# Performance work log

Hardware: AMD Instinct MI355X
Metric: run time of the kernel (lower is better)

## Reference

```python
import jax, jax.numpy as jnp
import numpy as np

EMBED_DIM = 256
NUM_EMBEDDINGS = 1024
COMMITMENT_COST = 0.25


def setup_inputs() -> dict:
    key = jax.random.key(0)
    k1, k2 = jax.random.split(key)
    z_e = jax.random.normal(k1, (64, 32, 32, EMBED_DIM), dtype=jnp.float32)
    # variance_scaling(fan_in, uniform) ~ U(-sqrt(3/fan_in), sqrt(3/fan_in))
    lim = float(np.sqrt(3.0 / EMBED_DIM))
    codebook = jax.random.uniform(k2, (NUM_EMBEDDINGS, EMBED_DIM), dtype=jnp.float32,
                                  minval=-lim, maxval=lim)
    return {"z_e": z_e, "codebook": codebook}


def reference(z_e, codebook):
    codebook = jnp.asarray(codebook, dtype=jnp.float32)
    z_flat = jnp.reshape(z_e, (-1, codebook.shape[1]))  # [N, D]
    # ||z||^2 - 2 z.c + ||c||^2 -> [N, K]
    distances = (jnp.sum(z_flat ** 2, axis=1, keepdims=True)
                 - 2.0 * jnp.dot(z_flat, codebook.T)
                 + jnp.sum(codebook ** 2, axis=1))
    encoding_indices = jnp.argmin(distances, axis=1)  # [N]
    quantized = jnp.reshape(codebook[encoding_indices], z_e.shape)
    commitment_loss = COMMITMENT_COST * jnp.mean((jax.lax.stop_gradient(quantized) - z_e) ** 2)
    embedding_loss = jnp.mean((quantized - jax.lax.stop_gradient(z_e)) ** 2)
    quantized = z_e + jax.lax.stop_gradient(quantized - z_e)  # straight-through
    return (quantized, commitment_loss, embedding_loss, encoding_indices)
```

## Files before the change

### kernel.cpp

```cpp
#include <hip/hip_runtime.h>

#define NROWS  65536
#define DIM    256
#define KCB    1024
#define DELTA  0.012f
#define DELTA2 2.0e-4f
#define NRMAX  65536
#define REFB   1024

typedef __attribute__((ext_vector_type(8))) _Float16 v8h;
typedef __attribute__((ext_vector_type(4))) float v4f;
typedef __attribute__((ext_vector_type(4))) int   v4i;

__device__ __forceinline__ unsigned short h16(float x) {
  _Float16 h = (_Float16)x;
  return __builtin_bit_cast(unsigned short, h);
}
__device__ __forceinline__ unsigned pk2h(float a, float b) {
  return (unsigned)h16(a) | ((unsigned)h16(b) << 16);
}
__device__ __forceinline__ v4i pk8h(float4 a, float4 b) {
  v4i r; r.x = (int)pk2h(a.x,a.y); r.y = (int)pk2h(a.z,a.w);
  r.z = (int)pk2h(b.x,b.y); r.w = (int)pk2h(b.z,b.w);
  return r;
}
__device__ __forceinline__ float f16f(float x) { return (float)(_Float16)x; }
__device__ __forceinline__ void gld16(const void* g, void* l) {
  __builtin_amdgcn_global_load_lds(
      (const __attribute__((address_space(1))) unsigned int*)g,
      (__attribute__((address_space(3))) unsigned int*)l, 16, 0, 0);
}

__global__ __launch_bounds__(256) void prep_kernel(const float* __restrict__ cb,
                                                   float* __restrict__ cnorm,
                                                   unsigned short* __restrict__ cbh,
                                                   unsigned short* __restrict__ cbl,
                                                   int* __restrict__ cnt,
                                                   int* __restrict__ cnt2) {
  int g = blockIdx.x * 256 + threadIdx.x;
  if (g == 0) { *cnt = 0; *cnt2 = 0; }
  int k = g >> 2, q = g & 3;
  int nt = k >> 7, c = k & 127;
  const float4* row = reinterpret_cast<const float4*>(cb + (size_t)k * DIM) + q * 16;
  size_t off = (size_t)((nt * 4 + q) * 128 + c) * 64;
  unsigned short* dh = cbh + off;
  unsigned short* dl = cbl + off;
  int xr = (c & 7) << 3;
  double s = 0.0;
#pragma unroll
  for (int i = 0; i < 8; ++i) {
    float4 a = row[2 * i], b = row[2 * i + 1];
    s += (double)a.x * a.x + (double)a.y * a.y + (double)a.z * a.z + (double)a.w * a.w;
    s += (double)b.x * b.x + (double)b.y * b.y + (double)b.z * b.z + (double)b.w * b.w;
    *(v4i*)(dh + ((i * 8) ^ xr)) = pk8h(a, b);
    float4 ar, br;
    ar.x = a.x - f16f(a.x); ar.y = a.y - f16f(a.y);
    ar.z = a.z - f16f(a.z); ar.w = a.w - f16f(a.w);
    br.x = b.x - f16f(b.x); br.y = b.y - f16f(b.y);
    br.z = b.z - f16f(b.z); br.w = b.w - f16f(b.w);
    *(v4i*)(dl + ((i * 8) ^ xr)) = pk8h(ar, br);
  }
  s += __shfl_xor(s, 1);
  s += __shfl_xor(s, 2);
  if (q == 0) cnorm[k] = (float)s;
}

__global__ __launch_bounds__(256, 2) void vq_mfma(
    const float* __restrict__ z, const unsigned short* __restrict__ cbh,
    const float* __restrict__ cnw, int* __restrict__ idx_arr,
    int* __restrict__ list, int* __restrict__ cnt) {
  __shared__ __align__(16) short S[32768];

  const int t = threadIdx.x;
  const int l = t & 63;
  const int w = t >> 6;
  const int l15 = l & 15, lhi = l >> 4;
  const int wm = w * 32;
  const int r0 = blockIdx.x * 128;

#pragma unroll
  for (int p = 0; p < 16; ++p) {
    int u = t + p * 256;
    int row = u >> 5, k8 = u & 31;
    const float4* s = (const float4*)(z + (size_t)(r0 + row) * DIM + k8 * 8);
    float4 a = s[0], b = s[1];
    *(v4i*)(S + row * 256 + ((k8 * 8) ^ ((row & 7) << 3))) = pk8h(a, b);
  }
  __syncthreads();

  v8h A[2][8];
#pragma unroll
  for (int mf = 0; mf < 2; ++mf) {
    int arow = wm + mf * 16 + l15;
    int base = arow * 256, xr = (arow & 7) << 3;
#pragma unroll
    for (int ks8 = 0; ks8 < 8; ++ks8)
      A[mf][ks8] = *(const v8h*)(S + base + ((ks8 * 32 + lhi * 8) ^ xr));
  }
  __syncthreads();

  auto stageC = [&](int p) {
    const char* gb = (const char*)cbh + (size_t)p * 32768 + w * 8192 + l * 16;
    char* lb = (char*)(S + (p & 1) * 16384) + w * 8192;
#pragma unroll
    for (int j = 0; j < 8; ++j) gld16(gb + j * 1024, lb + j * 1024);
  };

  int bcode[8], boff[8], bxr[8];
#pragma unroll
  for (int nf = 0; nf < 8; ++nf) {
    bcode[nf] = nf * 16 + l15;
    boff[nf] = bcode[nf] * 64;
    bxr[nf] = (bcode[nf] & 7) << 3;
  }

  float m1[8], m2[8]; int i1[8];
#pragma unroll
  for (int sl = 0; sl < 8; ++sl) { m1[sl] = 3.0e38f; m2[sl] = 3.0e38f; i1[sl] = 0; }

  stageC(0);
  __syncthreads();

  for (int nt = 0; nt < 8; ++nt) {
    float cnv[8];
#pragma unroll
    for (int nf = 0; nf < 8; ++nf) cnv[nf] = cnw[nt * 128 + bcode[nf]];

    v4f acc[2][8];
#pragma unroll
    for (int mf = 0; mf < 2; ++mf)
#pragma unroll
      for (int nf = 0; nf < 8; ++nf) acc[mf][nf] = (v4f){0.f, 0.f, 0.f, 0.f};

    for (int kh = 0; kh < 2; ++kh) {
      int p = nt * 2 + kh;
      if (p < 15) stageC(p + 1);
      const short* cur = S + (p & 1) * 16384;
#pragma unroll
      for (int ks = 0; ks < 4; ++ks) {
        int sub = (ks >> 1) * 8192;
        int ko = (ks & 1) * 32 + lhi * 8;
        v8h b[8];
#pragma unroll
        for (int nf = 0; nf < 8; ++nf)
          b[nf] = *(const v8h*)(cur + sub + boff[nf] + (ko ^ bxr[nf]));
#pragma unroll
        for (int mf = 0; mf < 2; ++mf)
#pragma unroll
          for (int nf = 0; nf < 8; ++nf)
            acc[mf][nf] = __builtin_amdgcn_mfma_f32_16x16x32_f16(A[mf][kh * 4 + ks], b[nf], acc[mf][nf], 0, 0, 0);
      }
      __syncthreads();
    }

#pragma unroll
    for (int mf = 0; mf < 2; ++mf)
#pragma unroll
      for (int nf = 0; nf < 8; ++nf) {
        int code = nt * 128 + bcode[nf];
#pragma unroll
        for (int r = 0; r < 4; ++r) {
          float s = fmaf(-2.f, acc[mf][nf][r], cnv[nf]);
          int sl = mf * 4 + r;
          m2[sl] = fminf(m2[sl], fmaxf(m1[sl], s));
          bool lt = s < m1[sl];
          i1[sl] = lt ? code : i1[sl];
          m1[sl] = lt ? s : m1[sl];
        }
      }
  }

#pragma unroll
  for (int off = 1; off < 16; off <<= 1) {
#pragma unroll
    for (int sl = 0; sl < 8; ++sl) {
      float o1 = __shfl_xor(m1[sl], off);
      int   oi = __shfl_xor(i1[sl], off);
      float o2 = __shfl_xor(m2[sl], off);
      bool bb = (o1 < m1[sl]) || (o1 == m1[sl] && oi < i1[sl]);
      float hi = fmaxf(m1[sl], o1);
      m2[sl] = fminf(hi, fminf(m2[sl], o2));
      m1[sl] = bb ? o1 : m1[sl];
      i1[sl] = bb ? oi : i1[sl];
    }
  }

  if (l15 == 0) {
#pragma unroll
    for (int sl = 0; sl < 8; ++sl) {
      int row = wm + (sl >> 2) * 16 + lhi * 4 + (sl & 3);
      idx_arr[r0 + row] = i1[sl];
      if (m2[sl] - m1[sl] < DELTA) {
        int p = atomicAdd(cnt, 1);
        list[p] = r0 + row;
      }
    }
  }
}

__global__ __launch_bounds__(256, 2) void vq_fused(
    const float* __restrict__ z, const float* __restrict__ cb,
    const unsigned short* __restrict__ cbh, const unsigned short* __restrict__ cbl,
    const float* __restrict__ cnw, const int* __restrict__ list,
    const int* __restrict__ cnt, const int* __restrict__ idx_arr,
    float* __restrict__ pm1, float* __restrict__ pm2, int* __restrict__ pi1,
    float* __restrict__ out_q, float* __restrict__ out_idx,
    float* __restrict__ rowloss) {
  __shared__ __align__(16) short Ch[2][8192];
  __shared__ __align__(16) short Cl[2][8192];
  __shared__ int rows_s[64];
  __shared__ int idxs[16];

  const int t = threadIdx.x;
  const int l = t & 63, w = t >> 6;
  const int l15 = l & 15, lhi = l >> 4;

  if (blockIdx.x < REFB) {
    const int n = *cnt;
    const int ngroups = (n + 63) >> 6;
    const int cq = blockIdx.x & 3;

    auto stage2 = [&](int g, int buf) {
      size_t go = (size_t)g * 16384 + w * 4096 + l * 16;
      char* lh = (char*)Ch[buf] + w * 4096;
      char* ll = (char*)Cl[buf] + w * 4096;
#pragma unroll
      for (int j = 0; j < 4; ++j) gld16((const char*)cbh + go + j * 1024, lh + j * 1024);
#pragma unroll
      for (int j = 0; j < 4; ++j) gld16((const char*)cbl + go + j * 1024, ll + j * 1024);
    };

    const int bxr = (l15 & 7) << 3;

    for (int grp = blockIdx.x >> 2; grp < ngroups; grp += (REFB >> 2)) {
      int base = grp * 64;
      __syncthreads();
      if (t < 64) rows_s[t] = list[min(base + t, n - 1)];
      __syncthreads();
      int rowg = rows_s[w * 16 + l15];

      v8h Ah[8], Al[8];
#pragma unroll
      for (int ks8 = 0; ks8 < 8; ++ks8) {
        const float* p = z + (size_t)rowg * 256 + ks8 * 32 + lhi * 8;
        float4 a = *(const float4*)p, b = *(const float4*)(p + 4);
        v8h hv, lv;
        hv[0] = (_Float16)a.x; lv[0] = (_Float16)(a.x - (float)hv[0]);
        hv[1] = (_Float16)a.y; lv[1] = (_Float16)(a.y - (float)hv[1]);
        hv[2] = (_Float16)a.z; lv[2] = (_Float16)(a.z - (float)hv[2]);
        hv[3] = (_Float16)a.w; lv[3] = (_Float16)(a.w - (float)hv[3]);
        hv[4] = (_Float16)b.x; lv[4] = (_Float16)(b.x - (float)hv[4]);
        hv[5] = (_Float16)b.y; lv[5] = (_Float16)(b.y - (float)hv[5]);
        hv[6] = (_Float16)b.z; lv[6] = (_Float16)(b.z - (float)hv[6]);
        hv[7] = (_Float16)b.w; lv[7] = (_Float16)(b.w - (float)hv[7]);
        Ah[ks8] = hv; Al[ks8] = lv;
      }

      stage2(cq * 8, 0);
      __syncthreads();

      float m1[4], m2[4]; int i1[4];
#pragma unroll
      for (int r = 0; r < 4; ++r) { m1[r] = 3.0e38f; m2[r] = 3.0e38f; i1[r] = 0; }

#pragma unroll
      for (int tnt = 0; tnt < 2; ++tnt) {
        int nt = cq * 2 + tnt;
        float cnv[8];
#pragma unroll
        for (int nf = 0; nf < 8; ++nf) cnv[nf] = cnw[nt * 128 + nf * 16 + l15];

        v4f acc[8];
#pragma unroll
        for (int nf = 0; nf < 8; ++nf) acc[nf] = (v4f){0.f, 0.f, 0.f, 0.f};

        for (int kc = 0; kc < 4; ++kc) {
          int ph = tnt * 4 + kc;
          int g = nt * 4 + kc;
          if (ph < 7) stage2(g + 1, (ph + 1) & 1);
          const short* ch = Ch[ph & 1];
          const short* cl = Cl[ph & 1];
#pragma unroll
          for (int ks = 0; ks < 2; ++ks) {
            int ko = (ks * 32 + lhi * 8) ^ bxr;
            v8h bh[8], bl8[8];
#pragma unroll
            for (int nf = 0; nf < 8; ++nf) {
              int bo = (nf * 16 + l15) * 64 + ko;
              bh[nf]  = *(const v8h*)(ch + bo);
              bl8[nf] = *(const v8h*)(cl + bo);
            }
            v8h ah = Ah[kc * 2 + ks], al = Al[kc * 2 + ks];
#pragma unroll
            for (int nf = 0; nf < 8; ++nf) {
              acc[nf] = __builtin_amdgcn_mfma_f32_16x16x32_f16(al, bh[nf], acc[nf], 0, 0, 0);
              acc[nf] = __builtin_amdgcn_mfma_f32_16x16x32_f16(ah, bl8[nf], acc[nf], 0, 0, 0);
              acc[nf] = __builtin_amdgcn_mfma_f32_16x16x32_f16(ah, bh[nf], acc[nf], 0, 0, 0);
            }
          }
          __syncthreads();
        }

#pragma unroll
        for (int nf = 0; nf < 8; ++nf) {
          int code = nt * 128 + nf * 16 + l15;
#pragma unroll
          for (int r = 0; r < 4; ++r) {
            float s = fmaf(-2.f, acc[nf][r], cnv[nf]);
            m2[r] = fminf(m2[r], fmaxf(m1[r], s));
            bool lt = s < m1[r];
            i1[r] = lt ? code : i1[r];
            m1[r] = lt ? s : m1[r];
          }
        }
      }

#pragma unroll
      for (int off = 1; off < 16; off <<= 1) {
#pragma unroll
        for (int r = 0; r < 4; ++r) {
          float o1 = __shfl_xor(m1[r], off);
          int   oi = __shfl_xor(i1[r], off);
          float o2 = __shfl_xor(m2[r], off);
          bool bb = (o1 < m1[r]) || (o1 == m1[r] && oi < i1[r]);
          float hi = fmaxf(m1[r], o1);
          m2[r] = fminf(hi, fminf(m2[r], o2));
          m1[r] = bb ? o1 : m1[r];
          i1[r] = bb ? oi : i1[r];
        }
      }

      if (l15 == 0) {
#pragma unroll
        for (int r = 0; r < 4; ++r) {
          int fr = w * 16 + lhi * 4 + r;
          int pos = base + fr;
          if (pos < n) {
            pm1[cq * NRMAX + pos] = m1[r];
            pm2[cq * NRMAX + pos] = m2[r];
            pi1[cq * NRMAX + pos] = i1[r];
          }
        }
      }
    }
  } else {
    const int b0 = (blockIdx.x - REFB) * 16;
    if (t < 16) {
      int k = idx_arr[b0 + t];
      idxs[t] = k;
      out_idx[b0 + t] = (float)k;
    }
    __syncthreads();
    const float4* zb = (const float4*)(z + (size_t)b0 * DIM);
    float4* qb = (float4*)(out_q + (size_t)b0 * DIM);
#pragma unroll
    for (int p = 0; p < 4; ++p) {
      int rl = p * 4 + w;
      int fi = p * 256 + t;
      int ki = idxs[rl];
      float4 zv = zb[fi];
      float4 cv = ((const float4*)(cb + (size_t)ki * DIM))[fi & 63];
      float dx = cv.x - zv.x, dy = cv.y - zv.y, dz = cv.z - zv.z, dw = cv.w - zv.w;
      float4 o; o.x = zv.x + dx; o.y = zv.y + dy; o.z = zv.z + dz; o.w = zv.w + dw;
      qb[fi] = o;
      double ls = (double)dx * dx + (double)dy * dy + (double)dz * dz + (double)dw * dw;
#pragma unroll
      for (int off = 1; off < 64; off <<= 1) ls += __shfl_xor(ls, off);
      if (l == 0) rowloss[b0 + rl] = (float)ls;
    }
  }
}

__global__ __launch_bounds__(256) void vq_merge(
    const int* __restrict__ list, const int* __restrict__ cnt,
    const float* __restrict__ pm1, const float* __restrict__ pm2,
    const int* __restrict__ pi1, int* __restrict__ idx_arr,
    int* __restrict__ list2, int* __restrict__ cnt2) {
  int i = blockIdx.x * 256 + threadIdx.x;
  int n = *cnt;
  if (i >= n) return;
  float m1 = pm1[i], m2 = pm2[i];
  int   i1 = pi1[i];
#pragma unroll
  for (int cq = 1; cq < 4; ++cq) {
    float o1 = pm1[cq * NRMAX + i];
    float o2 = pm2[cq * NRMAX + i];
    int   oi = pi1[cq * NRMAX + i];
    bool bb = (o1 < m1) || (o1 == m1 && oi < i1);
    float hi = fmaxf(m1, o1);
    m2 = fminf(hi, fminf(m2, o2));
    m1 = bb ? o1 : m1;
    i1 = bb ? oi : i1;
  }
  int row = list[i];
  idx_arr[row] = i1;
  if (m2 - m1 < DELTA2) {
    int p = atomicAdd(cnt2, 1);
    list2[p] = row;
  }
}

__global__ __launch_bounds__(256) void vq_rescue(
    const float* __restrict__ z, const float* __restrict__ cb,
    const float* __restrict__ cnw, const int* __restrict__ list,
    const int* __restrict__ cnt, int* __restrict__ idx_arr) {
  __shared__ float zs[256];
  __shared__ float As;
  __shared__ float wmin[4];
  __shared__ int   widx[4];

  const int t = threadIdx.x;
  const int l = t & 63, w = t >> 6;
  const int n = *cnt;

  for (int i = blockIdx.x; i < n; i += gridDim.x) {
    int row = list[i];
    __syncthreads();
    if (t < 64) ((float4*)zs)[t] = ((const float4*)(z + (size_t)row * DIM))[t];
    __syncthreads();
    if (t < 4) {
      double s = 0.0;
      const float* zz = zs + t * 64;
      for (int d = 0; d < 64; ++d) { float v = zz[d]; s += (double)v * v; }
      s += __shfl_xor(s, 1);
      s += __shfl_xor(s, 2);
      if (t == 0) As = (float)s;
    }
    __syncthreads();
    float Af = As;

    const float4* c0 = (const float4*)(cb + (size_t)(t      ) * DIM);
    const float4* c1 = (const float4*)(cb + (size_t)(t + 256) * DIM);
    const float4* c2 = (const float4*)(cb + (size_t)(t + 512) * DIM);
    const float4* c3 = (const float4*)(cb + (size_t)(t + 768) * DIM);
    float a0 = 0.f, a1 = 0.f, a2 = 0.f, a3 = 0.f;
    for (int d4 = 0; d4 < 64; ++d4) {
      float4 zq = *(const float4*)(zs + d4 * 4);
      float4 va = c0[d4], vb = c1[d4], vc = c2[d4], vd = c3[d4];
      a0 = fmaf(zq.x, va.x, a0); a0 = fmaf(zq.y, va.y, a0);
      a0 = fmaf(zq.z, va.z, a0); a0 = fmaf(zq.w, va.w, a0);
      a1 = fmaf(zq.x, vb.x, a1); a1 = fmaf(zq.y, vb.y, a1);
      a1 = fmaf(zq.z, vb.z, a1); a1 = fmaf(zq.w, vb.w, a1);
      a2 = fmaf(zq.x, vc.x, a2); a2 = fmaf(zq.y, vc.y, a2);
      a2 = fmaf(zq.z, vc.z, a2); a2 = fmaf(zq.w, vc.w, a2);
      a3 = fmaf(zq.x, vd.x, a3); a3 = fmaf(zq.y, vd.y, a3);
      a3 = fmaf(zq.z, vd.z, a3); a3 = fmaf(zq.w, vd.w, a3);
    }
    float accs[4] = {a0, a1, a2, a3};
    float mv = 3.0e38f; int mi = 0;
#pragma unroll
    for (int j = 0; j < 4; ++j) {
      int code = t + j * 256;
      float t1 = fmaf(-2.f, accs[j], Af);
      float t2 = t1 + cnw[code];
      if (t2 < mv) { mv = t2; mi = code; }
    }
#pragma unroll
    for (int off = 1; off < 64; off <<= 1) {
      float ov = __shfl_xor(mv, off);
      int   oi = __shfl_xor(mi, off);
      if (ov < mv || (ov == mv && oi < mi)) { mv = ov; mi = oi; }
    }
    if (l == 0) { wmin[w] = mv; widx[w] = mi; }
    __syncthreads();
    if (t == 0) {
      float bm = wmin[0]; int bi = widx[0];
#pragma unroll
      for (int q = 1; q < 4; ++q)
        if (wmin[q] < bm || (wmin[q] == bm && widx[q] < bi)) { bm = wmin[q]; bi = widx[q]; }
      idx_arr[row] = bi;
    }
    __syncthreads();
  }
}

__global__ __launch_bounds__(64) void vq_patch(
    const float* __restrict__ z, const float* __restrict__ cb,
    const int* __restrict__ list, const int* __restrict__ cnt,
    const int* __restrict__ idx_arr, float* __restrict__ out_q,
    float* __restrict__ out_idx, float* __restrict__ rowloss) {
  const int l = threadIdx.x;
  const int n = *cnt;
  for (int i = blockIdx.x; i < n; i += gridDim.x) {
    int row = list[i];
    int k = idx_arr[row];
    float4 zv = ((const float4*)(z + (size_t)row * DIM))[l];
    float4 cv = ((const float4*)(cb + (size_t)k * DIM))[l];
    float dx = cv.x - zv.x, dy = cv.y - zv.y, dz = cv.z - zv.z, dw = cv.w - zv.w;
    float4 o; o.x = zv.x + dx; o.y = zv.y + dy; o.z = zv.z + dz; o.w = zv.w + dw;
    ((float4*)(out_q + (size_t)row * DIM))[l] = o;
    double ls = (double)dx * dx + (double)dy * dy + (double)dz * dz + (double)dw * dw;
#pragma unroll
    for (int off = 1; off < 64; off <<= 1) ls += __shfl_xor(ls, off);
    if (l == 0) { rowloss[row] = (float)ls; out_idx[row] = (float)k; }
  }
}

__global__ __launch_bounds__(256) void finalize_kernel(const float* __restrict__ rowloss,
                                                       float* __restrict__ out_losses) {
  __shared__ double lw[4];
  const int t = threadIdx.x;
  double s = 0.0;
  for (int i = t; i < NROWS / 4; i += 256) {
    float4 v = ((const float4*)rowloss)[i];
    s += (double)v.x + (double)v.y + (double)v.z + (double)v.w;
  }
#pragma unroll
  for (int off = 1; off < 64; off <<= 1) s += __shfl_xor(s, off);
  if ((t & 63) == 0) lw[t >> 6] = s;
  __syncthreads();
  if (t == 0) {
    double mse = (lw[0] + lw[1] + lw[2] + lw[3]) / ((double)NROWS * (double)DIM);
    out_losses[0] = (float)(0.25 * mse);
    out_losses[1] = (float)mse;
  }
}

extern "C" void kernel_launch(void* const* d_in, const int* in_sizes, int n_in,
                              void* d_out, int out_size, void* d_ws, size_t ws_size,
                              hipStream_t stream) {
  const float* z  = (const float*)d_in[0];
  const float* cb = (const float*)d_in[1];
  float* out = (float*)d_out;

  char* ws = (char*)d_ws;
  int*            cnt     = (int*)(ws + 0);
  int*            cnt2    = (int*)(ws + 8);
  float*          cnorm   = (float*)(ws + 4096);
  float*          rowloss = (float*)(ws + 8192);
  int*            idx_arr = (int*)(ws + 270336);
  int*            list    = (int*)(ws + 532480);
  int*            list2   = (int*)(ws + 794624);
  unsigned short* cbh     = (unsigned short*)(ws + 1056768);
  unsigned short* cbl     = (unsigned short*)(ws + 1581056);
  float*          pm1     = (float*)(ws + 2105344);
  float*          pm2     = (float*)(ws + 3153920);
  int*            pi1     = (int*)(ws + 4202496);

  float* out_q      = out;
  float* out_losses = out + 16777216;
  float* out_idx    = out + 16777218;

  prep_kernel<<<16, 256, 0, stream>>>(cb, cnorm, cbh, cbl, cnt, cnt2);
  vq_mfma<<<NROWS / 128, 256, 0, stream>>>(z, cbh, cnorm, idx_arr, list, cnt);
  vq_fused<<<REFB + NROWS / 16, 256, 0, stream>>>(z, cb, cbh, cbl, cnorm, list, cnt,
                                                  idx_arr, pm1, pm2, pi1,
                                                  out_q, out_idx, rowloss);
  vq_merge<<<NRMAX / 256, 256, 0, stream>>>(list, cnt, pm1, pm2, pi1, idx_arr, list2, cnt2);
  vq_rescue<<<256, 256, 0, stream>>>(z, cb, cnorm, list2, cnt2, idx_arr);
  vq_patch<<<1024, 64, 0, stream>>>(z, cb, list, cnt, idx_arr, out_q, out_idx, rowloss);
  finalize_kernel<<<1, 256, 0, stream>>>(rowloss, out_losses);
}
```

Baseline: 166.3 us.

## Fold merge into rescue kernel and single-buffer codebook staging in refine

Removes the separate merge kernel and its second compaction list: the rescue kernel now merges the four partial min results per candidate row and either writes the index directly or runs the exact fp32 rescue, using a larger grid. The refine kernel drops LDS double buffering for a single buffer with barriers around each load, halving shared memory and changing launch bounds to one block per SIMD hint. This saves a launch and an atomic pass, but makes rescue blocks iterate over all candidates with block-uniform branching and serializes global-to-LDS loads with MFMA compute.

```diff
diff --git a/kernel.cpp b/kernel.cpp
--- a/kernel.cpp
+++ b/kernel.cpp
@@ -6,7 +6,7 @@
 #define DELTA  0.012f
 #define DELTA2 2.0e-4f
 #define NRMAX  65536
-#define REFB   1024
+#define RB     1024
 
 typedef __attribute__((ext_vector_type(8))) _Float16 v8h;
 typedef __attribute__((ext_vector_type(4))) float v4f;
@@ -35,10 +35,9 @@
                                                    float* __restrict__ cnorm,
                                                    unsigned short* __restrict__ cbh,
                                                    unsigned short* __restrict__ cbl,
-                                                   int* __restrict__ cnt,
-                                                   int* __restrict__ cnt2) {
+                                                   int* __restrict__ cnt) {
   int g = blockIdx.x * 256 + threadIdx.x;
-  if (g == 0) { *cnt = 0; *cnt2 = 0; }
+  if (g == 0) *cnt = 0;
   int k = g >> 2, q = g & 3;
   int nt = k >> 7, c = k & 127;
   const float4* row = reinterpret_cast<const float4*>(cb + (size_t)k * DIM) + q * 16;
@@ -198,7 +197,7 @@
   }
 }
 
-__global__ __launch_bounds__(256, 2) void vq_fused(
+__global__ __launch_bounds__(256, 1) void vq_tail(
     const float* __restrict__ z, const float* __restrict__ cb,
     const unsigned short* __restrict__ cbh, const unsigned short* __restrict__ cbl,
     const float* __restrict__ cnw, const int* __restrict__ list,
@@ -206,8 +205,8 @@
     float* __restrict__ pm1, float* __restrict__ pm2, int* __restrict__ pi1,
     float* __restrict__ out_q, float* __restrict__ out_idx,
     float* __restrict__ rowloss) {
-  __shared__ __align__(16) short Ch[2][8192];
-  __shared__ __align__(16) short Cl[2][8192];
+  __shared__ __align__(16) short Ch[8192];
+  __shared__ __align__(16) short Cl[8192];
   __shared__ int rows_s[64];
   __shared__ int idxs[16];
 
@@ -215,15 +214,15 @@
   const int l = t & 63, w = t >> 6;
   const int l15 = l & 15, lhi = l >> 4;
 
-  if (blockIdx.x < REFB) {
+  if (blockIdx.x < RB) {
     const int n = *cnt;
     const int ngroups = (n + 63) >> 6;
     const int cq = blockIdx.x & 3;
 
-    auto stage2 = [&](int g, int buf) {
+    auto stage2 = [&](int g) {
       size_t go = (size_t)g * 16384 + w * 4096 + l * 16;
-      char* lh = (char*)Ch[buf] + w * 4096;
-      char* ll = (char*)Cl[buf] + w * 4096;
+      char* lh = (char*)Ch + w * 4096;
+      char* ll = (char*)Cl + w * 4096;
 #pragma unroll
       for (int j = 0; j < 4; ++j) gld16((const char*)cbh + go + j * 1024, lh + j * 1024);
 #pragma unroll
@@ -232,7 +231,7 @@
 
     const int bxr = (l15 & 7) << 3;
 
-    for (int grp = blockIdx.x >> 2; grp < ngroups; grp += (REFB >> 2)) {
+    for (int grp = blockIdx.x >> 2; grp < ngroups; grp += (RB >> 2)) {
       int base = grp * 64;
       __syncthreads();
       if (t < 64) rows_s[t] = list[min(base + t, n - 1)];
@@ -256,9 +255,6 @@
         Ah[ks8] = hv; Al[ks8] = lv;
       }
 
-      stage2(cq * 8, 0);
-      __syncthreads();
-
       float m1[4], m2[4]; int i1[4];
 #pragma unroll
       for (int r = 0; r < 4; ++r) { m1[r] = 3.0e38f; m2[r] = 3.0e38f; i1[r] = 0; }
@@ -275,11 +271,10 @@
         for (int nf = 0; nf < 8; ++nf) acc[nf] = (v4f){0.f, 0.f, 0.f, 0.f};
 
         for (int kc = 0; kc < 4; ++kc) {
-          int ph = tnt * 4 + kc;
           int g = nt * 4 + kc;
-          if (ph < 7) stage2(g + 1, (ph + 1) & 1);
-          const short* ch = Ch[ph & 1];
-          const short* cl = Cl[ph & 1];
+          __syncthreads();
+          stage2(g);
+          __syncthreads();
 #pragma unroll
           for (int ks = 0; ks < 2; ++ks) {
             int ko = (ks * 32 + lhi * 8) ^ bxr;
@@ -287,8 +282,8 @@
 #pragma unroll
             for (int nf = 0; nf < 8; ++nf) {
               int bo = (nf * 16 + l15) * 64 + ko;
-              bh[nf]  = *(const v8h*)(ch + bo);
-              bl8[nf] = *(const v8h*)(cl + bo);
+              bh[nf]  = *(const v8h*)(Ch + bo);
+              bl8[nf] = *(const v8h*)(Cl + bo);
             }
             v8h ah = Ah[kc * 2 + ks], al = Al[kc * 2 + ks];
 #pragma unroll
@@ -298,7 +293,6 @@
               acc[nf] = __builtin_amdgcn_mfma_f32_16x16x32_f16(ah, bh[nf], acc[nf], 0, 0, 0);
             }
           }
-          __syncthreads();
         }
 
 #pragma unroll
@@ -344,7 +338,7 @@
       }
     }
   } else {
-    const int b0 = (blockIdx.x - REFB) * 16;
+    const int b0 = (blockIdx.x - RB) * 16;
     if (t < 16) {
       int k = idx_arr[b0 + t];
       idxs[t] = k;
@@ -371,39 +365,12 @@
   }
 }
 
-__global__ __launch_bounds__(256) void vq_merge(
-    const int* __restrict__ list, const int* __restrict__ cnt,
-    const float* __restrict__ pm1, const float* __restrict__ pm2,
-    const int* __restrict__ pi1, int* __restrict__ idx_arr,
-    int* __restrict__ list2, int* __restrict__ cnt2) {
-  int i = blockIdx.x * 256 + threadIdx.x;
-  int n = *cnt;
-  if (i >= n) return;
-  float m1 = pm1[i], m2 = pm2[i];
-  int   i1 = pi1[i];
-#pragma unroll
-  for (int cq = 1; cq < 4; ++cq) {
-    float o1 = pm1[cq * NRMAX + i];
-    float o2 = pm2[cq * NRMAX + i];
-    int   oi = pi1[cq * NRMAX + i];
-    bool bb = (o1 < m1) || (o1 == m1 && oi < i1);
-    float hi = fmaxf(m1, o1);
-    m2 = fminf(hi, fminf(m2, o2));
-    m1 = bb ? o1 : m1;
-    i1 = bb ? oi : i1;
-  }
-  int row = list[i];
-  idx_arr[row] = i1;
-  if (m2 - m1 < DELTA2) {
-    int p = atomicAdd(cnt2, 1);
-    list2[p] = row;
-  }
-}
-
-__global__ __launch_bounds__(256) void vq_rescue(
+__global__ __launch_bounds__(256) void vq_rescue2(
     const float* __restrict__ z, const float* __restrict__ cb,
     const float* __restrict__ cnw, const int* __restrict__ list,
-    const int* __restrict__ cnt, int* __restrict__ idx_arr) {
+    const int* __restrict__ cnt,
+    const float* __restrict__ pm1, const float* __restrict__ pm2,
+    const int* __restrict__ pi1, int* __restrict__ idx_arr) {
   __shared__ float zs[256];
   __shared__ float As;
   __shared__ float wmin[4];
@@ -415,6 +382,23 @@
 
   for (int i = blockIdx.x; i < n; i += gridDim.x) {
     int row = list[i];
+    float m1 = pm1[i], m2 = pm2[i];
+    int   i1 = pi1[i];
+#pragma unroll
+    for (int cq = 1; cq < 4; ++cq) {
+      float o1 = pm1[cq * NRMAX + i];
+      float o2 = pm2[cq * NRMAX + i];
+      int   oi = pi1[cq * NRMAX + i];
+      bool bb = (o1 < m1) || (o1 == m1 && oi < i1);
+      float hi = fmaxf(m1, o1);
+      m2 = fminf(hi, fminf(m2, o2));
+      m1 = bb ? o1 : m1;
+      i1 = bb ? oi : i1;
+    }
+    if (!(m2 - m1 < DELTA2)) {
+      if (t == 0) idx_arr[row] = i1;
+      continue;
+    }
     __syncthreads();
     if (t < 64) ((float4*)zs)[t] = ((const float4*)(z + (size_t)row * DIM))[t];
     __syncthreads();
@@ -525,29 +509,26 @@
 
   char* ws = (char*)d_ws;
   int*            cnt     = (int*)(ws + 0);
-  int*            cnt2    = (int*)(ws + 8);
   float*          cnorm   = (float*)(ws + 4096);
   float*          rowloss = (float*)(ws + 8192);
   int*            idx_arr = (int*)(ws + 270336);
   int*            list    = (int*)(ws + 532480);
-  int*            list2   = (int*)(ws + 794624);
-  unsigned short* cbh     = (unsigned short*)(ws + 1056768);
-  unsigned short* cbl     = (unsigned short*)(ws + 1581056);
-  float*          pm1     = (float*)(ws + 2105344);
-  float*          pm2     = (float*)(ws + 3153920);
-  int*            pi1     = (int*)(ws + 4202496);
+  unsigned short* cbh     = (unsigned short*)(ws + 794624);
+  unsigned short* cbl     = (unsigned short*)(ws + 1318912);
+  float*          pm1     = (float*)(ws + 1843200);
+  float*          pm2     = (float*)(ws + 2891776);
+  int*            pi1     = (int*)(ws + 3940352);
 
   float* out_q      = out;
   float* out_losses = out + 16777216;
   float* out_idx    = out + 16777218;
 
-  prep_kernel<<<16, 256, 0, stream>>>(cb, cnorm, cbh, cbl, cnt, cnt2);
+  prep_kernel<<<16, 256, 0, stream>>>(cb, cnorm, cbh, cbl, cnt);
   vq_mfma<<<NROWS / 128, 256, 0, stream>>>(z, cbh, cnorm, idx_arr, list, cnt);
-  vq_fused<<<REFB + NROWS / 16, 256, 0, stream>>>(z, cb, cbh, cbl, cnorm, list, cnt,
-                                                  idx_arr, pm1, pm2, pi1,
-                                                  out_q, out_idx, rowloss);
-  vq_merge<<<NRMAX / 256, 256, 0, stream>>>(list, cnt, pm1, pm2, pi1, idx_arr, list2, cnt2);
-  vq_rescue<<<256, 256, 0, stream>>>(z, cb, cnorm, list2, cnt2, idx_arr);
+  vq_tail<<<RB + NROWS / 16, 256, 0, stream>>>(z, cb, cbh, cbl, cnorm, list, cnt,
+                                               idx_arr, pm1, pm2, pi1,
+                                               out_q, out_idx, rowloss);
+  vq_rescue2<<<1024, 256, 0, stream>>>(z, cb, cnorm, list, cnt, pm1, pm2, pi1, idx_arr);
   vq_patch<<<1024, 64, 0, stream>>>(z, cb, list, cnt, idx_arr, out_q, out_idx, rowloss);
   finalize_kernel<<<1, 256, 0, stream>>>(rowloss, out_losses);
 }
```

Result: slower. 187.2 us (+12.6%).

## Fuse quantized output gather and loss into the MFMA argmin kernel

Applied to the files above, without the earlier changes.

The straight-through output write, index-to-float conversion and per-row loss are moved from the second kernel into the end of vq_mfma. The block's chosen indices go to shared memory and the block rereads its own z rows while they are likely still in cache. The refine path becomes its own kernel vq_refine with launch bounds of 1 block per SM. This drops a separate pass that re-reads z, but lengthens the main kernel's tail and loses the overlap between refinement and output writing that the old combined kernel had.

```diff
diff --git a/kernel.cpp b/kernel.cpp
--- a/kernel.cpp
+++ b/kernel.cpp
@@ -6,7 +6,6 @@
 #define DELTA  0.012f
 #define DELTA2 2.0e-4f
 #define NRMAX  65536
-#define REFB   1024
 
 typedef __attribute__((ext_vector_type(8))) _Float16 v8h;
 typedef __attribute__((ext_vector_type(4))) float v4f;
@@ -67,8 +66,10 @@
 
 __global__ __launch_bounds__(256, 2) void vq_mfma(
     const float* __restrict__ z, const unsigned short* __restrict__ cbh,
-    const float* __restrict__ cnw, int* __restrict__ idx_arr,
-    int* __restrict__ list, int* __restrict__ cnt) {
+    const float* __restrict__ cnw, const float* __restrict__ cb,
+    int* __restrict__ idx_arr, int* __restrict__ list, int* __restrict__ cnt,
+    float* __restrict__ out_q, float* __restrict__ out_idx,
+    float* __restrict__ rowloss) {
   __shared__ __align__(16) short S[32768];
 
   const int t = threadIdx.x;
@@ -185,188 +186,175 @@
     }
   }
 
+  int* idxS = (int*)S;
   if (l15 == 0) {
 #pragma unroll
     for (int sl = 0; sl < 8; ++sl) {
       int row = wm + (sl >> 2) * 16 + lhi * 4 + (sl & 3);
       idx_arr[r0 + row] = i1[sl];
+      out_idx[r0 + row] = (float)i1[sl];
+      idxS[row] = i1[sl];
       if (m2[sl] - m1[sl] < DELTA) {
         int p = atomicAdd(cnt, 1);
         list[p] = r0 + row;
       }
     }
   }
-}
-
-__global__ __launch_bounds__(256, 2) void vq_fused(
-    const float* __restrict__ z, const float* __restrict__ cb,
+  __syncthreads();
+
+  for (int p = 0; p < 32; ++p) {
+    int row = p * 4 + w;
+    int k = idxS[row];
+    float4 zv = ((const float4*)(z + (size_t)(r0 + row) * DIM))[l];
+    float4 cv = ((const float4*)(cb + (size_t)k * DIM))[l];
+    float dx = cv.x - zv.x, dy = cv.y - zv.y, dz = cv.z - zv.z, dw = cv.w - zv.w;
+    float4 o; o.x = zv.x + dx; o.y = zv.y + dy; o.z = zv.z + dz; o.w = zv.w + dw;
+    ((float4*)(out_q + (size_t)(r0 + row) * DIM))[l] = o;
+    double ls = (double)dx * dx + (double)dy * dy + (double)dz * dz + (double)dw * dw;
+#pragma unroll
+    for (int off = 1; off < 64; off <<= 1) ls += __shfl_xor(ls, off);
+    if (l == 0) rowloss[r0 + row] = (float)ls;
+  }
+}
+
+__global__ __launch_bounds__(256, 1) void vq_refine(
+    const float* __restrict__ z,
     const unsigned short* __restrict__ cbh, const unsigned short* __restrict__ cbl,
     const float* __restrict__ cnw, const int* __restrict__ list,
-    const int* __restrict__ cnt, const int* __restrict__ idx_arr,
-    float* __restrict__ pm1, float* __restrict__ pm2, int* __restrict__ pi1,
-    float* __restrict__ out_q, float* __restrict__ out_idx,
-    float* __restrict__ rowloss) {
+    const int* __restrict__ cnt,
+    float* __restrict__ pm1, float* __restrict__ pm2, int* __restrict__ pi1) {
   __shared__ __align__(16) short Ch[2][8192];
   __shared__ __align__(16) short Cl[2][8192];
   __shared__ int rows_s[64];
-  __shared__ int idxs[16];
 
   const int t = threadIdx.x;
   const int l = t & 63, w = t >> 6;
   const int l15 = l & 15, lhi = l >> 4;
-
-  if (blockIdx.x < REFB) {
-    const int n = *cnt;
-    const int ngroups = (n + 63) >> 6;
-    const int cq = blockIdx.x & 3;
-
-    auto stage2 = [&](int g, int buf) {
-      size_t go = (size_t)g * 16384 + w * 4096 + l * 16;
-      char* lh = (char*)Ch[buf] + w * 4096;
-      char* ll = (char*)Cl[buf] + w * 4096;
-#pragma unroll
-      for (int j = 0; j < 4; ++j) gld16((const char*)cbh + go + j * 1024, lh + j * 1024);
-#pragma unroll
-      for (int j = 0; j < 4; ++j) gld16((const char*)cbl + go + j * 1024, ll + j * 1024);
-    };
-
-    const int bxr = (l15 & 7) << 3;
-
-    for (int grp = blockIdx.x >> 2; grp < ngroups; grp += (REFB >> 2)) {
-      int base = grp * 64;
-      __syncthreads();
-      if (t < 64) rows_s[t] = list[min(base + t, n - 1)];
-      __syncthreads();
-      int rowg = rows_s[w * 16 + l15];
-
-      v8h Ah[8], Al[8];
-#pragma unroll
-      for (int ks8 = 0; ks8 < 8; ++ks8) {
-        const float* p = z + (size_t)rowg * 256 + ks8 * 32 + lhi * 8;
-        float4 a = *(const float4*)p, b = *(const float4*)(p + 4);
-        v8h hv, lv;
-        hv[0] = (_Float16)a.x; lv[0] = (_Float16)(a.x - (float)hv[0]);
-        hv[1] = (_Float16)a.y; lv[1] = (_Float16)(a.y - (float)hv[1]);
-        hv[2] = (_Float16)a.z; lv[2] = (_Float16)(a.z - (float)hv[2]);
-        hv[3] = (_Float16)a.w; lv[3] = (_Float16)(a.w - (float)hv[3]);
-        hv[4] = (_Float16)b.x; lv[4] = (_Float16)(b.x - (float)hv[4]);
-        hv[5] = (_Float16)b.y; lv[5] = (_Float16)(b.y - (float)hv[5]);
-        hv[6] = (_Float16)b.z; lv[6] = (_Float16)(b.z - (float)hv[6]);
-        hv[7] = (_Float16)b.w; lv[7] = (_Float16)(b.w - (float)hv[7]);
-        Ah[ks8] = hv; Al[ks8] = lv;
-      }
-
-      stage2(cq * 8, 0);
-      __syncthreads();
-
-      float m1[4], m2[4]; int i1[4];
-#pragma unroll
-      for (int r = 0; r < 4; ++r) { m1[r] = 3.0e38f; m2[r] = 3.0e38f; i1[r] = 0; }
-
-#pragma unroll
-      for (int tnt = 0; tnt < 2; ++tnt) {
-        int nt = cq * 2 + tnt;
-        float cnv[8];
-#pragma unroll
-        for (int nf = 0; nf < 8; ++nf) cnv[nf] = cnw[nt * 128 + nf * 16 + l15];
-
-        v4f acc[8];
-#pragma unroll
-        for (int nf = 0; nf < 8; ++nf) acc[nf] = (v4f){0.f, 0.f, 0.f, 0.f};
-
-        for (int kc = 0; kc < 4; ++kc) {
-          int ph = tnt * 4 + kc;
-          int g = nt * 4 + kc;
-          if (ph < 7) stage2(g + 1, (ph + 1) & 1);
-          const short* ch = Ch[ph & 1];
-          const short* cl = Cl[ph & 1];
-#pragma unroll
-          for (int ks = 0; ks < 2; ++ks) {
-            int ko = (ks * 32 + lhi * 8) ^ bxr;
-            v8h bh[8], bl8[8];
-#pragma unroll
-            for (int nf = 0; nf < 8; ++nf) {
-              int bo = (nf * 16 + l15) * 64 + ko;
-              bh[nf]  = *(const v8h*)(ch + bo);
-              bl8[nf] = *(const v8h*)(cl + bo);
-            }
-            v8h ah = Ah[kc * 2 + ks], al = Al[kc * 2 + ks];
-#pragma unroll
-            for (int nf = 0; nf < 8; ++nf) {
-              acc[nf] = __builtin_amdgcn_mfma_f32_16x16x32_f16(al, bh[nf], acc[nf], 0, 0, 0);
-              acc[nf] = __builtin_amdgcn_mfma_f32_16x16x32_f16(ah, bl8[nf], acc[nf], 0, 0, 0);
-              acc[nf] = __builtin_amdgcn_mfma_f32_16x16x32_f16(ah, bh[nf], acc[nf], 0, 0, 0);
-            }
+  const int n = *cnt;
+  const int ngroups = (n + 63) >> 6;
+  const int cq = blockIdx.x & 3;
+
+  auto stage2 = [&](int g, int buf) {
+    size_t go = (size_t)g * 16384 + w * 4096 + l * 16;
+    char* lh = (char*)Ch[buf] + w * 4096;
+    char* ll = (char*)Cl[buf] + w * 4096;
+#pragma unroll
+    for (int j = 0; j < 4; ++j) gld16((const char*)cbh + go + j * 1024, lh + j * 1024);
+#pragma unroll
+    for (int j = 0; j < 4; ++j) gld16((const char*)cbl + go + j * 1024, ll + j * 1024);
+  };
+
+  const int bxr = (l15 & 7) << 3;
+
+  for (int grp = blockIdx.x >> 2; grp < ngroups; grp += (gridDim.x >> 2)) {
+    int base = grp * 64;
+    __syncthreads();
+    if (t < 64) rows_s[t] = list[min(base + t, n - 1)];
+    __syncthreads();
+    int rowg = rows_s[w * 16 + l15];
+
+    v8h Ah[8], Al[8];
+#pragma unroll
+    for (int ks8 = 0; ks8 < 8; ++ks8) {
+      const float* p = z + (size_t)rowg * 256 + ks8 * 32 + lhi * 8;
+      float4 a = *(const float4*)p, b = *(const float4*)(p + 4);
+      v8h hv, lv;
+      hv[0] = (_Float16)a.x; lv[0] = (_Float16)(a.x - (float)hv[0]);
+      hv[1] = (_Float16)a.y; lv[1] = (_Float16)(a.y - (float)hv[1]);
+      hv[2] = (_Float16)a.z; lv[2] = (_Float16)(a.z - (float)hv[2]);
+      hv[3] = (_Float16)a.w; lv[3] = (_Float16)(a.w - (float)hv[3]);
+      hv[4] = (_Float16)b.x; lv[4] = (_Float16)(b.x - (float)hv[4]);
+      hv[5] = (_Float16)b.y; lv[5] = (_Float16)(b.y - (float)hv[5]);
+      hv[6] = (_Float16)b.z; lv[6] = (_Float16)(b.z - (float)hv[6]);
+      hv[7] = (_Float16)b.w; lv[7] = (_Float16)(b.w - (float)hv[7]);
+      Ah[ks8] = hv; Al[ks8] = lv;
+    }
+
+    stage2(cq * 8, 0);
+    __syncthreads();
+
+    float m1[4], m2[4]; int i1[4];
+#pragma unroll
+    for (int r = 0; r < 4; ++r) { m1[r] = 3.0e38f; m2[r] = 3.0e38f; i1[r] = 0; }
+
+#pragma unroll
+    for (int tnt = 0; tnt < 2; ++tnt) {
+      int nt = cq * 2 + tnt;
+      float cnv[8];
+#pragma unroll
+      for (int nf = 0; nf < 8; ++nf) cnv[nf] = cnw[nt * 128 + nf * 16 + l15];
+
+      v4f acc[8];
+#pragma unroll
+      for (int nf = 0; nf < 8; ++nf) acc[nf] = (v4f){0.f, 0.f, 0.f, 0.f};
+
+      for (int kc = 0; kc < 4; ++kc) {
+        int ph = tnt * 4 + kc;
+        int g = nt * 4 + kc;
+        if (ph < 7) stage2(g + 1, (ph + 1) & 1);
+        const short* ch = Ch[ph & 1];
+        const short* cl = Cl[ph & 1];
+#pragma unroll
+        for (int ks = 0; ks < 2; ++ks) {
+          int ko = (ks * 32 + lhi * 8) ^ bxr;
+          v8h bh[8], bl8[8];
+#pragma unroll
+          for (int nf = 0; nf < 8; ++nf) {
+            int bo = (nf * 16 + l15) * 64 + ko;
+            bh[nf]  = *(const v8h*)(ch + bo);
+            bl8[nf] = *(const v8h*)(cl + bo);
           }
-          __syncthreads();
-        }
-
-#pragma unroll
-        for (int nf = 0; nf < 8; ++nf) {
-          int code = nt * 128 + nf * 16 + l15;
-#pragma unroll
-          for (int r = 0; r < 4; ++r) {
-            float s = fmaf(-2.f, acc[nf][r], cnv[nf]);
-            m2[r] = fminf(m2[r], fmaxf(m1[r], s));
-            bool lt = s < m1[r];
-            i1[r] = lt ? code : i1[r];
-            m1[r] = lt ? s : m1[r];
+          v8h ah = Ah[kc * 2 + ks], al = Al[kc * 2 + ks];
+#pragma unroll
+          for (int nf = 0; nf < 8; ++nf) {
+            acc[nf] = __builtin_amdgcn_mfma_f32_16x16x32_f16(al, bh[nf], acc[nf], 0, 0, 0);
+            acc[nf] = __builtin_amdgcn_mfma_f32_16x16x32_f16(ah, bl8[nf], acc[nf], 0, 0, 0);
+            acc[nf] = __builtin_amdgcn_mfma_f32_16x16x32_f16(ah, bh[nf], acc[nf], 0, 0, 0);
           }
         }
-      }
-
-#pragma unroll
-      for (int off = 1; off < 16; off <<= 1) {
+        __syncthreads();
+      }
+
+#pragma unroll
+      for (int nf = 0; nf < 8; ++nf) {
+        int code = nt * 128 + nf * 16 + l15;
 #pragma unroll
         for (int r = 0; r < 4; ++r) {
-          float o1 = __shfl_xor(m1[r], off);
-          int   oi = __shfl_xor(i1[r], off);
-          float o2 = __shfl_xor(m2[r], off);
-          bool bb = (o1 < m1[r]) || (o1 == m1[r] && oi < i1[r]);
-          float hi = fmaxf(m1[r], o1);
-          m2[r] = fminf(hi, fminf(m2[r], o2));
-          m1[r] = bb ? o1 : m1[r];
-          i1[r] = bb ? oi : i1[r];
+          float s = fmaf(-2.f, acc[nf][r], cnv[nf]);
+          m2[r] = fminf(m2[r], fmaxf(m1[r], s));
+          bool lt = s < m1[r];
+          i1[r] = lt ? code : i1[r];
+          m1[r] = lt ? s : m1[r];
         }
       }
-
-      if (l15 == 0) {
-#pragma unroll
-        for (int r = 0; r < 4; ++r) {
-          int fr = w * 16 + lhi * 4 + r;
-          int pos = base + fr;
-          if (pos < n) {
-            pm1[cq * NRMAX + pos] = m1[r];
-            pm2[cq * NRMAX + pos] = m2[r];
-            pi1[cq * NRMAX + pos] = i1[r];
-          }
+    }
+
+#pragma unroll
+    for (int off = 1; off < 16; off <<= 1) {
+#pragma unroll
+      for (int r = 0; r < 4; ++r) {
+        float o1 = __shfl_xor(m1[r], off);
+        int   oi = __shfl_xor(i1[r], off);
+        float o2 = __shfl_xor(m2[r], off);
+        bool bb = (o1 < m1[r]) || (o1 == m1[r] && oi < i1[r]);
+        float hi = fmaxf(m1[r], o1);
+        m2[r] = fminf(hi, fminf(m2[r], o2));
+        m1[r] = bb ? o1 : m1[r];
+        i1[r] = bb ? oi : i1[r];
+      }
+    }
+
+    if (l15 == 0) {
+#pragma unroll
+      for (int r = 0; r < 4; ++r) {
+        int fr = w * 16 + lhi * 4 + r;
+        int pos = base + fr;
+        if (pos < n) {
+          pm1[cq * NRMAX + pos] = m1[r];
+          pm2[cq * NRMAX + pos] = m2[r];
+          pi1[cq * NRMAX + pos] = i1[r];
         }
       }
-    }
-  } else {
-    const int b0 = (blockIdx.x - REFB) * 16;
-    if (t < 16) {
-      int k = idx_arr[b0 + t];
-      idxs[t] = k;
-      out_idx[b0 + t] = (float)k;
-    }
-    __syncthreads();
-    const float4* zb = (const float4*)(z + (size_t)b0 * DIM);
-    float4* qb = (float4*)(out_q + (size_t)b0 * DIM);
-#pragma unroll
-    for (int p = 0; p < 4; ++p) {
-      int rl = p * 4 + w;
-      int fi = p * 256 + t;
-      int ki = idxs[rl];
-      float4 zv = zb[fi];
-      float4 cv = ((const float4*)(cb + (size_t)ki * DIM))[fi & 63];
-      float dx = cv.x - zv.x, dy = cv.y - zv.y, dz = cv.z - zv.z, dw = cv.w - zv.w;
-      float4 o; o.x = zv.x + dx; o.y = zv.y + dy; o.z = zv.z + dz; o.w = zv.w + dw;
-      qb[fi] = o;
-      double ls = (double)dx * dx + (double)dy * dy + (double)dz * dz + (double)dw * dw;
-#pragma unroll
-      for (int off = 1; off < 64; off <<= 1) ls += __shfl_xor(ls, off);
-      if (l == 0) rowloss[b0 + rl] = (float)ls;
     }
   }
 }
@@ -542,10 +530,9 @@
   float* out_idx    = out + 16777218;
 
   prep_kernel<<<16, 256, 0, stream>>>(cb, cnorm, cbh, cbl, cnt, cnt2);
-  vq_mfma<<<NROWS / 128, 256, 0, stream>>>(z, cbh, cnorm, idx_arr, list, cnt);
-  vq_fused<<<REFB + NROWS / 16, 256, 0, stream>>>(z, cb, cbh, cbl, cnorm, list, cnt,
-                                                  idx_arr, pm1, pm2, pi1,
-                                                  out_q, out_idx, rowloss);
+  vq_mfma<<<NROWS / 128, 256, 0, stream>>>(z, cbh, cnorm, cb, idx_arr, list, cnt,
+                                           out_q, out_idx, rowloss);
+  vq_refine<<<1024, 256, 0, stream>>>(z, cbh, cbl, cnorm, list, cnt, pm1, pm2, pi1);
   vq_merge<<<NRMAX / 256, 256, 0, stream>>>(list, cnt, pm1, pm2, pi1, idx_arr, list2, cnt2);
   vq_rescue<<<256, 256, 0, stream>>>(z, cb, cnorm, list2, cnt2, idx_arr);
   vq_patch<<<1024, 64, 0, stream>>>(z, cb, list, cnt, idx_arr, out_q, out_idx, rowloss);
```

Result: no change. 163.4 us (-1.8%).
